# Kernel tuning notes

Hardware: AMD Instinct MI355X
Metric: run time of the kernel (lower is better)

## Reference

```python
import jax, jax.numpy as jnp
import numpy as np

B, S, D = 2, 2048, 1024
H = 16
HD = D // H
MINUS_INFINITY = -1000000000.0


def setup_inputs() -> dict:
    key = jax.random.key(0)
    ks = jax.random.split(key, 6)
    sc = 0.02
    return {
        "x": jax.random.normal(ks[0], (B, S, D), dtype=jnp.float32),
        "Wq": jax.random.normal(ks[1], (D, D), dtype=jnp.float32) * sc,
        "Wk": jax.random.normal(ks[2], (D, D), dtype=jnp.float32) * sc,
        "Wv": jax.random.normal(ks[3], (D, D), dtype=jnp.float32) * sc,
        "Wo": jax.random.normal(ks[4], (D, D), dtype=jnp.float32) * sc,
        "bo": jnp.zeros((D,), dtype=jnp.float32),
    }


def reference(x, Wq, Wk, Wv, Wo, bo):
    b, n, _ = x.shape
    # Linear with transpose_b=True: x @ W.T
    q = jnp.einsum('bnd,ed->bne', x, Wq).reshape(b, n, H, HD).transpose(0, 2, 1, 3)
    k = jnp.einsum('bnd,ed->bne', x, Wk).reshape(b, n, H, HD).transpose(0, 2, 1, 3)
    v = jnp.einsum('bnd,ed->bne', x, Wv).reshape(b, n, H, HD).transpose(0, 2, 1, 3)
    scores = jnp.einsum('bhqd,bhkd->bhqk', q, k) * (1.0 / HD ** 0.5)
    mask = jnp.triu(jnp.ones((n, n), dtype=scores.dtype), k=1) * MINUS_INFINITY
    scores = scores + mask[None, None, :, :]
    attn = jax.nn.softmax(scores, axis=-1)  # dropout prob = 0.0
    ctx = jnp.einsum('bhqk,bhkd->bhqd', attn, v)
    ctx = ctx.transpose(0, 2, 1, 3).reshape(b, n, D)
    return jnp.einsum('bnd,ed->bne', ctx, Wo) + bo
```

## Files before the change

### kernel.cpp

```cpp
#include <hip/hip_runtime.h>
#include <hip/hip_bf16.h>

#define B_  2
#define S_  2048
#define D_  1024
#define H_  16
#define HD_ 64

typedef __attribute__((ext_vector_type(8))) short short8;
typedef __attribute__((ext_vector_type(4))) float f32x4;

__device__ __forceinline__ unsigned short f2b(float f) {
    __hip_bfloat16 h = __float2bfloat16(f);
    unsigned short u;
    __builtin_memcpy(&u, &h, 2);
    return u;
}

__global__ __launch_bounds__(256) void convert_kernel(
    const float* __restrict__ x,  const float* __restrict__ Wq,
    const float* __restrict__ Wk, const float* __restrict__ Wv,
    const float* __restrict__ Wo, unsigned short* __restrict__ dst)
{
    const long long i4 = blockIdx.x * 256 + threadIdx.x;
    const long long e  = i4 * 4;
    const long long M1 = 1048576LL;
    const float* src;
    if      (e < 4 * M1) src = x  + e;
    else if (e < 5 * M1) src = Wq + (e - 4 * M1);
    else if (e < 6 * M1) src = Wk + (e - 5 * M1);
    else if (e < 7 * M1) src = Wv + (e - 6 * M1);
    else                 src = Wo + (e - 7 * M1);
    float4 v = *(const float4*)src;
    unsigned long long pk = (unsigned long long)f2b(v.x)
                          | ((unsigned long long)f2b(v.y) << 16)
                          | ((unsigned long long)f2b(v.z) << 32)
                          | ((unsigned long long)f2b(v.w) << 48);
    *(unsigned long long*)&dst[e] = pk;
}

__global__ __launch_bounds__(256) void qkv_proj_kernel(
    const unsigned short* __restrict__ x,
    const unsigned short* __restrict__ Wq,
    const unsigned short* __restrict__ Wk,
    const unsigned short* __restrict__ Wv,
    unsigned short* __restrict__ q_ws,
    unsigned short* __restrict__ k_ws,
    unsigned short* __restrict__ vT_ws)
{
    __shared__ unsigned short a_lds[128][72];
    __shared__ unsigned short b_lds[128][72];

    const int m0 = blockIdx.x * 128;
    const int n0 = blockIdx.y * 128;
    const int which = blockIdx.z;
    const unsigned short* W = (which == 0) ? Wq : (which == 1) ? Wk : Wv;

    const int tid  = threadIdx.x;
    const int wave = tid >> 6;
    const int lane = tid & 63;
    const int l15  = lane & 15;
    const int quad = lane >> 4;
    const int wm = (wave & 1) * 64;
    const int wn = (wave >> 1) * 64;

    f32x4 acc[4][4];
    #pragma unroll
    for (int sm = 0; sm < 4; ++sm)
        #pragma unroll
        for (int sn = 0; sn < 4; ++sn)
            #pragma unroll
            for (int r = 0; r < 4; ++r) acc[sm][sn][r] = 0.f;

    const int row = tid >> 3;
    const int c8  = tid & 7;

    for (int kk = 0; kk < D_; kk += 64) {
        #pragma unroll
        for (int rp = 0; rp < 4; ++rp) {
            *(uint4*)&a_lds[row + rp * 32][c8 * 8] =
                *(const uint4*)&x[(m0 + row + rp * 32) * D_ + kk + c8 * 8];
            *(uint4*)&b_lds[row + rp * 32][c8 * 8] =
                *(const uint4*)&W[(n0 + row + rp * 32) * D_ + kk + c8 * 8];
        }
        __syncthreads();
        #pragma unroll
        for (int kc = 0; kc < 2; ++kc) {
            short8 af[4], bf[4];
            #pragma unroll
            for (int s = 0; s < 4; ++s) {
                af[s] = *(const short8*)&a_lds[wm + s * 16 + l15][kc * 32 + quad * 8];
                bf[s] = *(const short8*)&b_lds[wn + s * 16 + l15][kc * 32 + quad * 8];
            }
            #pragma unroll
            for (int sm = 0; sm < 4; ++sm)
                #pragma unroll
                for (int sn = 0; sn < 4; ++sn)
                    acc[sm][sn] = __builtin_amdgcn_mfma_f32_16x16x32_bf16(
                        af[sm], bf[sn], acc[sm][sn], 0, 0, 0);
        }
        __syncthreads();
    }

    #pragma unroll
    for (int sm = 0; sm < 4; ++sm) {
        #pragma unroll
        for (int sn = 0; sn < 4; ++sn) {
            const int n  = n0 + wn + sn * 16 + l15;
            const int h  = n >> 6;
            const int hd = n & 63;
            const int mbase = m0 + wm + sm * 16 + quad * 4;
            const int b     = mbase >> 11;
            const int sbase = mbase & 2047;
            if (which == 2) {
                unsigned long long pk = 0;
                #pragma unroll
                for (int r = 0; r < 4; ++r)
                    pk |= (unsigned long long)f2b(acc[sm][sn][r]) << (16 * r);
                *(unsigned long long*)&vT_ws[((b * H_ + h) * HD_ + hd) * S_ + sbase] = pk;
            } else if (which == 0) {
                #pragma unroll
                for (int r = 0; r < 4; ++r)
                    q_ws[((b * H_ + h) * S_ + (sbase + r)) * HD_ + hd] =
                        f2b(acc[sm][sn][r] * 0.125f);
            } else {
                #pragma unroll
                for (int r = 0; r < 4; ++r)
                    k_ws[((b * H_ + h) * S_ + (sbase + r)) * HD_ + hd] =
                        f2b(acc[sm][sn][r]);
            }
        }
    }
}

__global__ __launch_bounds__(256) void attn_kernel(
    const unsigned short* __restrict__ q_ws,
    const unsigned short* __restrict__ k_ws,
    const unsigned short* __restrict__ vT_ws,
    unsigned short* __restrict__ ctx_ws)
{
    __shared__ unsigned short k_lds[2][64][72];
    __shared__ unsigned short vT_lds[2][64][72];
    __shared__ unsigned short q_lds[64][72];
    __shared__ unsigned short p_lds[4][16][72];

    const int pair = blockIdx.x;
    const int bh   = blockIdx.y;

    const int tid  = threadIdx.x;
    const int wave = tid >> 6;
    const int lane = tid & 63;
    const int l15  = lane & 15;
    const int quad = lane >> 4;
    const int row  = tid >> 3;
    const int c8   = tid & 7;

    const unsigned short* Qh = q_ws + bh * (S_ * HD_);
    const unsigned short* Kh = k_ws + bh * (S_ * HD_);
    const unsigned short* Vt = vT_ws + bh * (HD_ * S_);
    const int b = bh >> 4;
    const int h = bh & 15;

    #pragma unroll
    for (int ph = 0; ph < 2; ++ph) {
        const int qt = (ph == 0) ? (31 - pair) : pair;
        const int q0 = qt * 64;
        const int qrow_base = q0 + wave * 16 + quad * 4;

        __syncthreads();
        *(uint4*)&q_lds[row][c8 * 8]      = *(const uint4*)&Qh[(q0 + row) * HD_ + c8 * 8];
        *(uint4*)&q_lds[row + 32][c8 * 8] = *(const uint4*)&Qh[(q0 + row + 32) * HD_ + c8 * 8];
        *(uint4*)&k_lds[0][row][c8 * 8]       = *(const uint4*)&Kh[row * HD_ + c8 * 8];
        *(uint4*)&k_lds[0][row + 32][c8 * 8]  = *(const uint4*)&Kh[(row + 32) * HD_ + c8 * 8];
        *(uint4*)&vT_lds[0][row][c8 * 8]      = *(const uint4*)&Vt[row * S_ + c8 * 8];
        *(uint4*)&vT_lds[0][row + 32][c8 * 8] = *(const uint4*)&Vt[(row + 32) * S_ + c8 * 8];
        __syncthreads();

        short8 aq[2];
        aq[0] = *(const short8*)&q_lds[wave * 16 + l15][quad * 8];
        aq[1] = *(const short8*)&q_lds[wave * 16 + l15][32 + quad * 8];

        float M[4], l_lane[4];
        f32x4 o[4];
        #pragma unroll
        for (int r = 0; r < 4; ++r) { M[r] = -1e30f; l_lane[r] = 0.f; }
        #pragma unroll
        for (int f = 0; f < 4; ++f)
            #pragma unroll
            for (int r = 0; r < 4; ++r) o[f][r] = 0.f;

        for (int kt = 0; kt <= qt; ++kt) {
            const int cur = kt & 1;
            if (kt < qt) {
                const int nk0 = (kt + 1) * 64;
                const int nb  = cur ^ 1;
                *(uint4*)&k_lds[nb][row][c8 * 8]       = *(const uint4*)&Kh[(nk0 + row) * HD_ + c8 * 8];
                *(uint4*)&k_lds[nb][row + 32][c8 * 8]  = *(const uint4*)&Kh[(nk0 + row + 32) * HD_ + c8 * 8];
                *(uint4*)&vT_lds[nb][row][c8 * 8]      = *(const uint4*)&Vt[row * S_ + nk0 + c8 * 8];
                *(uint4*)&vT_lds[nb][row + 32][c8 * 8] = *(const uint4*)&Vt[(row + 32) * S_ + nk0 + c8 * 8];
            }

            f32x4 sc[4];
            #pragma unroll
            for (int f = 0; f < 4; ++f)
                #pragma unroll
                for (int r = 0; r < 4; ++r) sc[f][r] = 0.f;
            #pragma unroll
            for (int f = 0; f < 4; ++f)
                #pragma unroll
                for (int kc = 0; kc < 2; ++kc) {
                    short8 bk = *(const short8*)&k_lds[cur][f * 16 + l15][kc * 32 + quad * 8];
                    sc[f] = __builtin_amdgcn_mfma_f32_16x16x32_bf16(aq[kc], bk, sc[f], 0, 0, 0);
                }

            float p[4][4], mloc[4];
            if (kt == qt) {
                const int k0 = kt * 64;
                #pragma unroll
                for (int f = 0; f < 4; ++f) {
                    const int kg = k0 + f * 16 + l15;
                    #pragma unroll
                    for (int r = 0; r < 4; ++r)
                        p[f][r] = (kg > qrow_base + r) ? -1e30f : sc[f][r];
                }
            } else {
                #pragma unroll
                for (int f = 0; f < 4; ++f)
                    #pragma unroll
                    for (int r = 0; r < 4; ++r) p[f][r] = sc[f][r];
            }

            #pragma unroll
            for (int r = 0; r < 4; ++r)
                mloc[r] = fmaxf(fmaxf(p[0][r], p[1][r]), fmaxf(p[2][r], p[3][r]));
            #pragma unroll
            for (int off = 1; off < 16; off <<= 1)
                #pragma unroll
                for (int r = 0; r < 4; ++r)
                    mloc[r] = fmaxf(mloc[r], __shfl_xor(mloc[r], off, 64));

            float alpha[4];
            #pragma unroll
            for (int r = 0; r < 4; ++r) {
                float Mn = fmaxf(M[r], mloc[r]);
                alpha[r] = __expf(M[r] - Mn);
                M[r] = Mn;
            }
            #pragma unroll
            for (int f = 0; f < 4; ++f)
                #pragma unroll
                for (int r = 0; r < 4; ++r)
                    p[f][r] = __expf(p[f][r] - M[r]);
            #pragma unroll
            for (int r = 0; r < 4; ++r)
                l_lane[r] = l_lane[r] * alpha[r]
                          + ((p[0][r] + p[1][r]) + (p[2][r] + p[3][r]));

            #pragma unroll
            for (int f = 0; f < 4; ++f)
                #pragma unroll
                for (int r = 0; r < 4; ++r)
                    p_lds[wave][quad * 4 + r][f * 16 + l15] = f2b(p[f][r]);

            #pragma unroll
            for (int f = 0; f < 4; ++f)
                #pragma unroll
                for (int r = 0; r < 4; ++r)
                    o[f][r] *= alpha[r];

            short8 ap[2];
            ap[0] = *(const short8*)&p_lds[wave][l15][quad * 8];
            ap[1] = *(const short8*)&p_lds[wave][l15][32 + quad * 8];
            #pragma unroll
            for (int f = 0; f < 4; ++f)
                #pragma unroll
                for (int kc = 0; kc < 2; ++kc) {
                    short8 bv = *(const short8*)&vT_lds[cur][f * 16 + l15][kc * 32 + quad * 8];
                    o[f] = __builtin_amdgcn_mfma_f32_16x16x32_bf16(ap[kc], bv, o[f], 0, 0, 0);
                }

            __syncthreads();
        }

        float l[4];
        #pragma unroll
        for (int r = 0; r < 4; ++r) l[r] = l_lane[r];
        #pragma unroll
        for (int off = 1; off < 16; off <<= 1)
            #pragma unroll
            for (int r = 0; r < 4; ++r)
                l[r] += __shfl_xor(l[r], off, 64);

        #pragma unroll
        for (int f = 0; f < 4; ++f) {
            const int col = h * 64 + f * 16 + l15;
            #pragma unroll
            for (int r = 0; r < 4; ++r) {
                const int qg = qrow_base + r;
                ctx_ws[(b * S_ + qg) * D_ + col] = f2b(o[f][r] / l[r]);
            }
        }
    }
}

__global__ __launch_bounds__(256) void out_proj_kernel(
    const unsigned short* __restrict__ ctx,
    const unsigned short* __restrict__ Wo,
    const float* __restrict__ bo,
    float* __restrict__ out)
{
    __shared__ unsigned short a_lds[128][72];
    __shared__ unsigned short b_lds[128][72];

    const int m0 = blockIdx.x * 128;
    const int n0 = blockIdx.y * 128;

    const int tid  = threadIdx.x;
    const int wave = tid >> 6;
    const int lane = tid & 63;
    const int l15  = lane & 15;
    const int quad = lane >> 4;
    const int wm = (wave & 1) * 64;
    const int wn = (wave >> 1) * 64;

    f32x4 acc[4][4];
    #pragma unroll
    for (int sm = 0; sm < 4; ++sm)
        #pragma unroll
        for (int sn = 0; sn < 4; ++sn)
            #pragma unroll
            for (int r = 0; r < 4; ++r) acc[sm][sn][r] = 0.f;

    const int row = tid >> 3;
    const int c8  = tid & 7;

    for (int kk = 0; kk < D_; kk += 64) {
        #pragma unroll
        for (int rp = 0; rp < 4; ++rp) {
            *(uint4*)&a_lds[row + rp * 32][c8 * 8] =
                *(const uint4*)&ctx[(m0 + row + rp * 32) * D_ + kk + c8 * 8];
            *(uint4*)&b_lds[row + rp * 32][c8 * 8] =
                *(const uint4*)&Wo[(n0 + row + rp * 32) * D_ + kk + c8 * 8];
        }
        __syncthreads();
        #pragma unroll
        for (int kc = 0; kc < 2; ++kc) {
            short8 af[4], bf[4];
            #pragma unroll
            for (int s = 0; s < 4; ++s) {
                af[s] = *(const short8*)&a_lds[wm + s * 16 + l15][kc * 32 + quad * 8];
                bf[s] = *(const short8*)&b_lds[wn + s * 16 + l15][kc * 32 + quad * 8];
            }
            #pragma unroll
            for (int sm = 0; sm < 4; ++sm)
                #pragma unroll
                for (int sn = 0; sn < 4; ++sn)
                    acc[sm][sn] = __builtin_amdgcn_mfma_f32_16x16x32_bf16(
                        af[sm], bf[sn], acc[sm][sn], 0, 0, 0);
        }
        __syncthreads();
    }

    #pragma unroll
    for (int sm = 0; sm < 4; ++sm) {
        #pragma unroll
        for (int sn = 0; sn < 4; ++sn) {
            const int n = n0 + wn + sn * 16 + l15;
            const float bias = bo[n];
            const int mbase = m0 + wm + sm * 16 + quad * 4;
            #pragma unroll
            for (int r = 0; r < 4; ++r)
                out[(mbase + r) * D_ + n] = acc[sm][sn][r] + bias;
        }
    }
}

extern "C" void kernel_launch(void* const* d_in, const int* in_sizes, int n_in,
                              void* d_out, int out_size, void* d_ws, size_t ws_size,
                              hipStream_t stream) {
    const float* x  = (const float*)d_in[0];
    const float* Wq = (const float*)d_in[1];
    const float* Wk = (const float*)d_in[2];
    const float* Wv = (const float*)d_in[3];
    const float* Wo = (const float*)d_in[4];
    const float* bo = (const float*)d_in[5];
    float* out = (float*)d_out;

    const size_t M1 = 1048576;
    const size_t SZ = 4 * M1;

    unsigned short* xb  = (unsigned short*)d_ws;
    unsigned short* wqb = xb  + SZ;
    unsigned short* wkb = wqb + M1;
    unsigned short* wvb = wkb + M1;
    unsigned short* wob = wvb + M1;
    unsigned short* q_ws   = wob + M1;
    unsigned short* k_ws   = q_ws + SZ;
    unsigned short* vT_ws  = k_ws + SZ;
    unsigned short* ctx_ws = vT_ws + SZ;

    convert_kernel<<<dim3(8192), 256, 0, stream>>>(x, Wq, Wk, Wv, Wo, xb);
    qkv_proj_kernel<<<dim3(32, 8, 3), 256, 0, stream>>>(xb, wqb, wkb, wvb, q_ws, k_ws, vT_ws);
    attn_kernel<<<dim3(16, 32), 256, 0, stream>>>(q_ws, k_ws, vT_ws, ctx_ws);
    out_proj_kernel<<<dim3(32, 8), 256, 0, stream>>>(ctx_ws, wob, bo, out);
}
```

Measured before the change: 202.7 us.

## Use direct global-to-LDS loads with XOR swizzle and register-resident attention probabilities

The projection GEMMs now stage tiles with global_load_lds (direct global-to-LDS DMA) into an unpadded, XOR-swizzled layout, replacing the register round-trip and padded arrays. The attention kernel swaps the MFMA operand order so each lane owns one query row, which simplifies the max and sum reductions to two shuffles. The P tile is passed to the PV MFMA through cross-lane shuffles instead of an LDS round-trip, and context output is written with packed 8-byte stores. These target LDS traffic, register staging and reduction overhead. The cost is added shuffle work and reliance on the swizzle matching the DMA write pattern, and there is still no double buffering in the GEMM loop.

```diff
diff --git a/kernel.cpp b/kernel.cpp
--- a/kernel.cpp
+++ b/kernel.cpp
@@ -15,6 +15,12 @@
     unsigned short u;
     __builtin_memcpy(&u, &h, 2);
     return u;
+}
+
+__device__ __forceinline__ void gl_lds16(const unsigned short* g, unsigned short* l) {
+    __builtin_amdgcn_global_load_lds(
+        (const __attribute__((address_space(1))) unsigned int*)g,
+        (__attribute__((address_space(3))) unsigned int*)l, 16, 0, 0);
 }
 
 __global__ __launch_bounds__(256) void convert_kernel(
@@ -39,6 +45,23 @@
     *(unsigned long long*)&dst[e] = pk;
 }
 
+__device__ __forceinline__ void stage_tile_128x64(
+    const unsigned short* __restrict__ gbase,
+    unsigned short* lds, int wave, int lane)
+{
+    const int r8 = lane >> 3;
+    const int cb = (lane & 7) ^ r8;
+    #pragma unroll
+    for (int t = 0; t < 4; ++t) {
+        const int row = (wave * 4 + t) * 8 + r8;
+        gl_lds16(gbase + row * D_ + cb * 8, lds + (wave * 4 + t) * 512);
+    }
+}
+
+__device__ __forceinline__ short8 frag_ld(const unsigned short* lds, int row, int cbk) {
+    return *(const short8*)&lds[(row * 8 + (cbk ^ (row & 7))) * 8];
+}
+
 __global__ __launch_bounds__(256) void qkv_proj_kernel(
     const unsigned short* __restrict__ x,
     const unsigned short* __restrict__ Wq,
@@ -48,8 +71,8 @@
     unsigned short* __restrict__ k_ws,
     unsigned short* __restrict__ vT_ws)
 {
-    __shared__ unsigned short a_lds[128][72];
-    __shared__ unsigned short b_lds[128][72];
+    __shared__ unsigned short a_lds[128 * 64];
+    __shared__ unsigned short b_lds[128 * 64];
 
     const int m0 = blockIdx.x * 128;
     const int n0 = blockIdx.y * 128;
@@ -72,25 +95,17 @@
             #pragma unroll
             for (int r = 0; r < 4; ++r) acc[sm][sn][r] = 0.f;
 
-    const int row = tid >> 3;
-    const int c8  = tid & 7;
-
     for (int kk = 0; kk < D_; kk += 64) {
-        #pragma unroll
-        for (int rp = 0; rp < 4; ++rp) {
-            *(uint4*)&a_lds[row + rp * 32][c8 * 8] =
-                *(const uint4*)&x[(m0 + row + rp * 32) * D_ + kk + c8 * 8];
-            *(uint4*)&b_lds[row + rp * 32][c8 * 8] =
-                *(const uint4*)&W[(n0 + row + rp * 32) * D_ + kk + c8 * 8];
-        }
+        stage_tile_128x64(x + m0 * D_ + kk, a_lds, wave, lane);
+        stage_tile_128x64(W + n0 * D_ + kk, b_lds, wave, lane);
         __syncthreads();
         #pragma unroll
         for (int kc = 0; kc < 2; ++kc) {
             short8 af[4], bf[4];
             #pragma unroll
             for (int s = 0; s < 4; ++s) {
-                af[s] = *(const short8*)&a_lds[wm + s * 16 + l15][kc * 32 + quad * 8];
-                bf[s] = *(const short8*)&b_lds[wn + s * 16 + l15][kc * 32 + quad * 8];
+                af[s] = frag_ld(a_lds, wm + s * 16 + l15, kc * 4 + quad);
+                bf[s] = frag_ld(b_lds, wn + s * 16 + l15, kc * 4 + quad);
             }
             #pragma unroll
             for (int sm = 0; sm < 4; ++sm)
@@ -142,7 +157,6 @@
     __shared__ unsigned short k_lds[2][64][72];
     __shared__ unsigned short vT_lds[2][64][72];
     __shared__ unsigned short q_lds[64][72];
-    __shared__ unsigned short p_lds[4][16][72];
 
     const int pair = blockIdx.x;
     const int bh   = blockIdx.y;
@@ -161,11 +175,15 @@
     const int b = bh >> 4;
     const int h = bh & 15;
 
+    const int src0 = l15 + 32 * (quad & 1);
+    const int src1 = src0 + 16;
+    const int sel  = quad >> 1;
+
     #pragma unroll
     for (int ph = 0; ph < 2; ++ph) {
         const int qt = (ph == 0) ? (31 - pair) : pair;
         const int q0 = qt * 64;
-        const int qrow_base = q0 + wave * 16 + quad * 4;
+        const int qg = q0 + wave * 16 + l15;
 
         __syncthreads();
         *(uint4*)&q_lds[row][c8 * 8]      = *(const uint4*)&Qh[(q0 + row) * HD_ + c8 * 8];
@@ -180,10 +198,8 @@
         aq[0] = *(const short8*)&q_lds[wave * 16 + l15][quad * 8];
         aq[1] = *(const short8*)&q_lds[wave * 16 + l15][32 + quad * 8];
 
-        float M[4], l_lane[4];
+        float M = -1e30f, l_lane = 0.f;
         f32x4 o[4];
-        #pragma unroll
-        for (int r = 0; r < 4; ++r) { M[r] = -1e30f; l_lane[r] = 0.f; }
         #pragma unroll
         for (int f = 0; f < 4; ++f)
             #pragma unroll
@@ -209,20 +225,18 @@
             for (int f = 0; f < 4; ++f)
                 #pragma unroll
                 for (int kc = 0; kc < 2; ++kc) {
-                    short8 bk = *(const short8*)&k_lds[cur][f * 16 + l15][kc * 32 + quad * 8];
-                    sc[f] = __builtin_amdgcn_mfma_f32_16x16x32_bf16(aq[kc], bk, sc[f], 0, 0, 0);
+                    short8 ak = *(const short8*)&k_lds[cur][f * 16 + l15][kc * 32 + quad * 8];
+                    sc[f] = __builtin_amdgcn_mfma_f32_16x16x32_bf16(ak, aq[kc], sc[f], 0, 0, 0);
                 }
 
-            float p[4][4], mloc[4];
+            float p[4][4];
             if (kt == qt) {
-                const int k0 = kt * 64;
-                #pragma unroll
-                for (int f = 0; f < 4; ++f) {
-                    const int kg = k0 + f * 16 + l15;
+                const int kbase = kt * 64 + quad * 4;
+                #pragma unroll
+                for (int f = 0; f < 4; ++f)
                     #pragma unroll
                     for (int r = 0; r < 4; ++r)
-                        p[f][r] = (kg > qrow_base + r) ? -1e30f : sc[f][r];
-                }
+                        p[f][r] = (kbase + f * 16 + r > qg) ? -1e30f : sc[f][r];
             } else {
                 #pragma unroll
                 for (int f = 0; f < 4; ++f)
@@ -230,75 +244,77 @@
                     for (int r = 0; r < 4; ++r) p[f][r] = sc[f][r];
             }
 
+            float mloc = -1e30f;
+            #pragma unroll
+            for (int f = 0; f < 4; ++f)
+                #pragma unroll
+                for (int r = 0; r < 4; ++r) mloc = fmaxf(mloc, p[f][r]);
+            mloc = fmaxf(mloc, __shfl_xor(mloc, 16, 64));
+            mloc = fmaxf(mloc, __shfl_xor(mloc, 32, 64));
+
+            const float Mn = fmaxf(M, mloc);
+            const float alpha = __expf(M - Mn);
+            M = Mn;
+
+            float rs = 0.f;
+            #pragma unroll
+            for (int f = 0; f < 4; ++f)
+                #pragma unroll
+                for (int r = 0; r < 4; ++r) {
+                    p[f][r] = __expf(p[f][r] - M);
+                    rs += p[f][r];
+                }
+            l_lane = l_lane * alpha + rs;
+
+            #pragma unroll
+            for (int f = 0; f < 4; ++f)
+                #pragma unroll
+                for (int r = 0; r < 4; ++r) o[f][r] *= alpha;
+
+            unsigned int pd[4][2];
+            #pragma unroll
+            for (int f = 0; f < 4; ++f) {
+                pd[f][0] = (unsigned int)f2b(p[f][0]) | ((unsigned int)f2b(p[f][1]) << 16);
+                pd[f][1] = (unsigned int)f2b(p[f][2]) | ((unsigned int)f2b(p[f][3]) << 16);
+            }
+
+            #pragma unroll
+            for (int c = 0; c < 2; ++c) {
+                const int a0 = __shfl((int)pd[c * 2][0],     src0, 64);
+                const int a1 = __shfl((int)pd[c * 2][1],     src0, 64);
+                const int a2 = __shfl((int)pd[c * 2][0],     src1, 64);
+                const int a3 = __shfl((int)pd[c * 2][1],     src1, 64);
+                const int b0 = __shfl((int)pd[c * 2 + 1][0], src0, 64);
+                const int b1 = __shfl((int)pd[c * 2 + 1][1], src0, 64);
+                const int b2 = __shfl((int)pd[c * 2 + 1][0], src1, 64);
+                const int b3 = __shfl((int)pd[c * 2 + 1][1], src1, 64);
+                union { int i[4]; short8 s; } u;
+                u.i[0] = sel ? b0 : a0;
+                u.i[1] = sel ? b1 : a1;
+                u.i[2] = sel ? b2 : a2;
+                u.i[3] = sel ? b3 : a3;
+                #pragma unroll
+                for (int f = 0; f < 4; ++f) {
+                    short8 av = *(const short8*)&vT_lds[cur][f * 16 + l15][c * 32 + quad * 8];
+                    o[f] = __builtin_amdgcn_mfma_f32_16x16x32_bf16(av, u.s, o[f], 0, 0, 0);
+                }
+            }
+
+            __syncthreads();
+        }
+
+        float l = l_lane;
+        l += __shfl_xor(l, 16, 64);
+        l += __shfl_xor(l, 32, 64);
+        const float inv_l = 1.0f / l;
+
+        #pragma unroll
+        for (int f = 0; f < 4; ++f) {
+            unsigned long long pk = 0;
             #pragma unroll
             for (int r = 0; r < 4; ++r)
-                mloc[r] = fmaxf(fmaxf(p[0][r], p[1][r]), fmaxf(p[2][r], p[3][r]));
-            #pragma unroll
-            for (int off = 1; off < 16; off <<= 1)
-                #pragma unroll
-                for (int r = 0; r < 4; ++r)
-                    mloc[r] = fmaxf(mloc[r], __shfl_xor(mloc[r], off, 64));
-
-            float alpha[4];
-            #pragma unroll
-            for (int r = 0; r < 4; ++r) {
-                float Mn = fmaxf(M[r], mloc[r]);
-                alpha[r] = __expf(M[r] - Mn);
-                M[r] = Mn;
-            }
-            #pragma unroll
-            for (int f = 0; f < 4; ++f)
-                #pragma unroll
-                for (int r = 0; r < 4; ++r)
-                    p[f][r] = __expf(p[f][r] - M[r]);
-            #pragma unroll
-            for (int r = 0; r < 4; ++r)
-                l_lane[r] = l_lane[r] * alpha[r]
-                          + ((p[0][r] + p[1][r]) + (p[2][r] + p[3][r]));
-
-            #pragma unroll
-            for (int f = 0; f < 4; ++f)
-                #pragma unroll
-                for (int r = 0; r < 4; ++r)
-                    p_lds[wave][quad * 4 + r][f * 16 + l15] = f2b(p[f][r]);
-
-            #pragma unroll
-            for (int f = 0; f < 4; ++f)
-                #pragma unroll
-                for (int r = 0; r < 4; ++r)
-                    o[f][r] *= alpha[r];
-
-            short8 ap[2];
-            ap[0] = *(const short8*)&p_lds[wave][l15][quad * 8];
-            ap[1] = *(const short8*)&p_lds[wave][l15][32 + quad * 8];
-            #pragma unroll
-            for (int f = 0; f < 4; ++f)
-                #pragma unroll
-                for (int kc = 0; kc < 2; ++kc) {
-                    short8 bv = *(const short8*)&vT_lds[cur][f * 16 + l15][kc * 32 + quad * 8];
-                    o[f] = __builtin_amdgcn_mfma_f32_16x16x32_bf16(ap[kc], bv, o[f], 0, 0, 0);
-                }
-
-            __syncthreads();
-        }
-
-        float l[4];
-        #pragma unroll
-        for (int r = 0; r < 4; ++r) l[r] = l_lane[r];
-        #pragma unroll
-        for (int off = 1; off < 16; off <<= 1)
-            #pragma unroll
-            for (int r = 0; r < 4; ++r)
-                l[r] += __shfl_xor(l[r], off, 64);
-
-        #pragma unroll
-        for (int f = 0; f < 4; ++f) {
-            const int col = h * 64 + f * 16 + l15;
-            #pragma unroll
-            for (int r = 0; r < 4; ++r) {
-                const int qg = qrow_base + r;
-                ctx_ws[(b * S_ + qg) * D_ + col] = f2b(o[f][r] / l[r]);
-            }
+                pk |= (unsigned long long)f2b(o[f][r] * inv_l) << (16 * r);
+            *(unsigned long long*)&ctx_ws[(b * S_ + qg) * D_ + h * 64 + f * 16 + quad * 4] = pk;
         }
     }
 }
@@ -309,8 +325,8 @@
     const float* __restrict__ bo,
     float* __restrict__ out)
 {
-    __shared__ unsigned short a_lds[128][72];
-    __shared__ unsigned short b_lds[128][72];
+    __shared__ unsigned short a_lds[128 * 64];
+    __shared__ unsigned short b_lds[128 * 64];
 
     const int m0 = blockIdx.x * 128;
     const int n0 = blockIdx.y * 128;
@@ -331,25 +347,17 @@
             #pragma unroll
             for (int r = 0; r < 4; ++r) acc[sm][sn][r] = 0.f;
 
-    const int row = tid >> 3;
-    const int c8  = tid & 7;
-
     for (int kk = 0; kk < D_; kk += 64) {
-        #pragma unroll
-        for (int rp = 0; rp < 4; ++rp) {
-            *(uint4*)&a_lds[row + rp * 32][c8 * 8] =
-                *(const uint4*)&ctx[(m0 + row + rp * 32) * D_ + kk + c8 * 8];
-            *(uint4*)&b_lds[row + rp * 32][c8 * 8] =
-                *(const uint4*)&Wo[(n0 + row + rp * 32) * D_ + kk + c8 * 8];
-        }
+        stage_tile_128x64(ctx + m0 * D_ + kk, a_lds, wave, lane);
+        stage_tile_128x64(Wo + n0 * D_ + kk, b_lds, wave, lane);
         __syncthreads();
         #pragma unroll
         for (int kc = 0; kc < 2; ++kc) {
             short8 af[4], bf[4];
             #pragma unroll
             for (int s = 0; s < 4; ++s) {
-                af[s] = *(const short8*)&a_lds[wm + s * 16 + l15][kc * 32 + quad * 8];
-                bf[s] = *(const short8*)&b_lds[wn + s * 16 + l15][kc * 32 + quad * 8];
+                af[s] = frag_ld(a_lds, wm + s * 16 + l15, kc * 4 + quad);
+                bf[s] = frag_ld(b_lds, wn + s * 16 + l15, kc * 4 + quad);
             }
             #pragma unroll
             for (int sm = 0; sm < 4; ++sm)
```

Result: no change. 205.6 us (+1.4%).
